# Performance work log

Hardware: AMD Instinct MI355X
Metric: run time of the kernel (lower is better)

The kernel has to match this reference:

```python
import jax, jax.numpy as jnp
import numpy as np

B, N, E = 32, 128, 16384
D, H, O, A = 72, 72, 72, 4   # n_input, n_hidden, n_output, n_node_attr
C_WEIGHT = 1.0
EPS = 1e-5  # BatchNorm1d default eps


def setup_inputs() -> dict:
    key = jax.random.key(0)
    ks = jax.random.split(key, 16)
    rn = lambda k, shp, s=0.05: jax.random.normal(k, shp, jnp.float32) * s
    return {
        "h": jax.random.normal(ks[0], (B, N, D), jnp.float32),
        "x": jax.random.normal(ks[1], (B, N, 4), jnp.float32),
        "edgei": jax.random.randint(ks[2], (B, E), 0, N),
        "edgej": jax.random.randint(ks[3], (B, E), 0, N),
        "node_attr": jax.random.normal(ks[4], (B, N, A), jnp.float32),
        # phi_e: Linear(2D+2 -> H, no bias), BN, ReLU, Linear(H->H), ReLU
        "We1": rn(ks[5], (2 * D + 2, H)),
        "g1": jnp.ones((H,), jnp.float32), "b1": jnp.zeros((H,), jnp.float32),
        "We2": rn(ks[6], (H, H)), "be2": jnp.zeros((H,), jnp.float32),
        # phi_m: Linear(H->1), Sigmoid
        "Wm": rn(ks[7], (H, 1)), "bm": jnp.zeros((1,), jnp.float32),
        # phi_x: Linear(H->H), ReLU, Linear(H->1, no bias, tiny init)
        "Wx1": rn(ks[8], (H, H)), "bx1": jnp.zeros((H,), jnp.float32),
        "Wx2": rn(ks[9], (H, 1), 0.001),
        # phi_h: Linear(H+D+A -> H), BN, ReLU, Linear(H->O)
        "Wh1": rn(ks[10], (H + D + A, H)), "bh1": jnp.zeros((H,), jnp.float32),
        "gh": jnp.ones((H,), jnp.float32), "bh": jnp.zeros((H,), jnp.float32),
        "Wh2": rn(ks[11], (H, O)), "bh2": jnp.zeros((O,), jnp.float32),
    }


def _psi(p):
    return jnp.sign(p) * jnp.log1p(jnp.abs(p))


def _normsq4(p):  # Minkowski norm: p0^2 - p1^2 - p2^2 - p3^2
    psq = p * p
    return 2.0 * psq[..., 0] - psq.sum(axis=-1)


def _dotsq4(p, q):  # Minkowski inner product
    pq = p * q
    return 2.0 * pq[..., 0] - pq.sum(axis=-1)


def _batchnorm(z, g, b):  # training-mode BatchNorm1d over flattened batch dim
    mu = z.mean(axis=0)
    var = z.var(axis=0)
    return (z - mu) * jax.lax.rsqrt(var + EPS) * g + b


_seg_sum = jax.vmap(lambda d, s: jax.ops.segment_sum(d, s, num_segments=N))


def reference(h, x, edgei, edgej, node_attr,
              We1, g1, b1, We2, be2, Wm, bm,
              Wx1, bx1, Wx2, Wh1, bh1, gh, bh, Wh2, bh2):
    # gather edge endpoint features (equiv. to torch.gather along dim 1)
    xi = jnp.take_along_axis(x, edgei[:, :, None], axis=1)    # [B,E,4]
    xj = jnp.take_along_axis(x, edgej[:, :, None], axis=1)
    hi = jnp.take_along_axis(h, edgei[:, :, None], axis=1)    # [B,E,D]
    hj = jnp.take_along_axis(h, edgej[:, :, None], axis=1)
    x_diff = xi - xj
    norms = _psi(_normsq4(x_diff))[..., None]                 # [B,E,1]
    dots = _psi(_dotsq4(xi, xj))[..., None]                   # [B,E,1]

    # m_model: phi_e then sigmoid gate phi_m
    feat = jnp.concatenate([hi, hj, norms, dots], axis=-1)    # [B,E,2D+2]
    z = feat.reshape(-1, 2 * D + 2) @ We1
    z = jax.nn.relu(_batchnorm(z, g1, b1))
    z = jax.nn.relu(z @ We2 + be2)
    m = z.reshape(B, E, H)
    m = m * jax.nn.sigmoid(m @ Wm + bm)                       # gated messages

    # x_model: equivariant coordinate update (segment mean over edges)
    gate = jax.nn.relu(m @ Wx1 + bx1) @ Wx2                   # [B,E,1]
    trans = jnp.clip(x_diff * gate, -100.0, 100.0)
    agg = _seg_sum(trans, edgei)                              # [B,N,4]
    cnt = _seg_sum(jnp.ones_like(trans), edgei)
    x_out = x + (agg / jnp.maximum(cnt, 1.0)) * C_WEIGHT

    # h_model: segment sum of messages, node MLP, residual
    magg = _seg_sum(m, edgei)                                 # [B,N,H]
    hin = jnp.concatenate([h, magg, node_attr], axis=-1).reshape(-1, H + D + A)
    z2 = hin @ Wh1 + bh1
    z2 = jax.nn.relu(_batchnorm(z2, gh, bh))
    z2 = z2 @ Wh2 + bh2
    h_out = h + z2.reshape(B, N, O)

    return (h_out, x_out, m)
```

## Files before the change

### kernel.cpp

```cpp
#include <hip/hip_runtime.h>

#define BB 32
#define NN 128
#define EE 16384
#define ROWS_E (BB*EE)
#define ROWS_N (BB*NN)
#define EPS_BN 1e-5f

#define XOUT_OFF (ROWS_N*72)
#define M_OFF    (XOUT_OFF + ROWS_N*4)

#define ST1_OFF 0
#define ST2_OFF 512
#define AGG_OFF 1024
#define CNT_OFF (AGG_OFF + ROWS_N*4)
#define MAGG_OFF (CNT_OFF + ROWS_N)
#define Z2_OFF (MAGG_OFF + ROWS_N*72)
#define ZERO_FLOATS Z2_OFF
#define WB_OFF (Z2_OFF + ROWS_N*72)

#define WE1T_OFF 0
#define WE2T_OFF 13440
#define WX1T_OFF 21760
#define WH1T_OFF 30080
#define WH2T_OFF 43520
#define WB_TOTAL 51840

typedef __attribute__((ext_vector_type(8))) short short8;
typedef __attribute__((ext_vector_type(4))) float f32x4;

__device__ __forceinline__ float psi_f(float p) {
    return copysignf(log1pf(fabsf(p)), p);
}
__device__ __forceinline__ unsigned short f2bf(float f) {
    union { float f; unsigned u; } v; v.f = f;
    unsigned r = v.u + 0x7fffu + ((v.u >> 16) & 1u);
    return (unsigned short)(r >> 16);
}
__device__ __forceinline__ unsigned pk(float a, float b) {
    return (unsigned)f2bf(a) | ((unsigned)f2bf(b) << 16);
}

__global__ void k_prep(const float* __restrict__ We1, const float* __restrict__ We2,
                       const float* __restrict__ Wx1, const float* __restrict__ Wh1,
                       const float* __restrict__ Wh2, unsigned short* __restrict__ wb)
{
    int idx = blockIdx.x * 256 + threadIdx.x;
    if (idx >= WB_TOTAL) return;
    const float* src; int off, n, k, K;
    if (idx < WE2T_OFF)      { off = idx;            n = off/168; k = off%168; src = We1; K = 146; }
    else if (idx < WH1T_OFF && idx >= WX1T_OFF) { off = idx - WX1T_OFF; n = off/104; k = off%104; src = Wx1; K = 72; }
    else if (idx < WX1T_OFF) { off = idx - WE2T_OFF; n = off/104; k = off%104; src = We2; K = 72; }
    else if (idx < WH2T_OFF) { off = idx - WH1T_OFF; n = off/168; k = off%168; src = Wh1; K = 148; }
    else                     { off = idx - WH2T_OFF; n = off/104; k = off%104; src = Wh2; K = 72; }
    float v = (n < 72 && k < K) ? src[k * 72 + n] : 0.f;
    wb[idx] = f2bf(v);
}

__global__ __launch_bounds__(256) void k_edge_gemm1(
    const float* __restrict__ h, const float* __restrict__ x,
    const int* __restrict__ ei, const int* __restrict__ ej,
    const unsigned short* __restrict__ We1t, float* __restrict__ z1)
{
    __shared__ unsigned short At[128 * 168];
    __shared__ unsigned short Wt[80 * 168];
    int tid = threadIdx.x;
    {
        const uint4* s = (const uint4*)We1t; uint4* d = (uint4*)Wt;
        for (int q = tid; q < 1680; q += 256) d[q] = s[q];
    }
    int rl = tid >> 1, half = tid & 1;
    int row = blockIdx.x * 128 + rl;
    int b = row >> 14;
    int i = ei[row], j = ej[row];
    int node = half ? j : i;
    const float4* hp = (const float4*)(h + (size_t)(b * 128 + node) * 72);
    uint2* arow = (uint2*)(&At[rl * 168 + half * 72]);
    #pragma unroll
    for (int q = 0; q < 18; q++) {
        float4 v = hp[q];
        arow[q] = make_uint2(pk(v.x, v.y), pk(v.z, v.w));
    }
    unsigned* tailp = (unsigned*)(&At[rl * 168 + 146]);
    if (half == 0) {
        float4 xi = *(const float4*)(x + (size_t)(b * 128 + i) * 4);
        float4 xj = *(const float4*)(x + (size_t)(b * 128 + j) * 4);
        float d0 = xi.x - xj.x, d1 = xi.y - xj.y, d2 = xi.z - xj.z, d3 = xi.w - xj.w;
        float nrm = d0*d0 - d1*d1 - d2*d2 - d3*d3;
        float dot = xi.x*xj.x - xi.y*xj.y - xi.z*xj.z - xi.w*xj.w;
        *(unsigned*)(&At[rl * 168 + 144]) = pk(psi_f(nrm), psi_f(dot));
        #pragma unroll
        for (int q = 0; q < 6; q++) tailp[q] = 0u;
    } else {
        #pragma unroll
        for (int q = 6; q < 11; q++) tailp[q] = 0u;
    }
    __syncthreads();

    int wv = tid >> 6, lane = tid & 63, c = lane & 15, quad = lane >> 4;
    f32x4 acc[2][5] = {};
    for (int kc = 0; kc < 5; kc++) {
        int k0 = kc * 32 + quad * 8;
        short8 a0 = *(const short8*)(&At[(wv * 32 + c) * 168 + k0]);
        short8 a1 = *(const short8*)(&At[(wv * 32 + 16 + c) * 168 + k0]);
        #pragma unroll
        for (int ct = 0; ct < 5; ct++) {
            short8 bf = *(const short8*)(&Wt[(ct * 16 + c) * 168 + k0]);
            acc[0][ct] = __builtin_amdgcn_mfma_f32_16x16x32_bf16(a0, bf, acc[0][ct], 0, 0, 0);
            acc[1][ct] = __builtin_amdgcn_mfma_f32_16x16x32_bf16(a1, bf, acc[1][ct], 0, 0, 0);
        }
    }
    size_t rbase = (size_t)blockIdx.x * 128 + wv * 32 + quad * 4;
    #pragma unroll
    for (int rt = 0; rt < 2; rt++)
        #pragma unroll
        for (int ct = 0; ct < 5; ct++) {
            int col = ct * 16 + c;
            if (col < 72) {
                float* op = z1 + (rbase + rt * 16) * 72 + col;
                #pragma unroll
                for (int r = 0; r < 4; r++) op[(size_t)r * 72] = acc[rt][ct][r];
            }
        }
}

__global__ void k_stats(const float* __restrict__ z, int rows, float* __restrict__ st)
{
    __shared__ float ssum[4][72];
    __shared__ float ssq[4][72];
    int c = threadIdx.x, ty = threadIdx.y;
    float s = 0.f, q = 0.f;
    for (int r = blockIdx.x * 4 + ty; r < rows; r += gridDim.x * 4) {
        float v = z[(size_t)r * 72 + c];
        s += v; q += v * v;
    }
    ssum[ty][c] = s; ssq[ty][c] = q;
    __syncthreads();
    if (ty == 0) {
        s = ssum[0][c] + ssum[1][c] + ssum[2][c] + ssum[3][c];
        q = ssq[0][c] + ssq[1][c] + ssq[2][c] + ssq[3][c];
        atomicAdd(&st[c], s);
        atomicAdd(&st[72 + c], q);
    }
}

__global__ void k_finalize(float* __restrict__ st, float inv_rows)
{
    int c = threadIdx.x;
    if (c < 72) {
        float mean = st[c] * inv_rows;
        float var  = st[72 + c] * inv_rows - mean * mean;
        st[144 + c] = mean;
        st[216 + c] = rsqrtf(var + EPS_BN);
    }
}

__global__ __launch_bounds__(256) void k_edge_main(
    const float* __restrict__ x, const int* __restrict__ ei, const int* __restrict__ ej,
    const float* __restrict__ st1, const float* __restrict__ g1, const float* __restrict__ b1,
    const float* __restrict__ be2, const float* __restrict__ Wm, const float* __restrict__ bm,
    const float* __restrict__ bx1, const float* __restrict__ Wx2,
    const unsigned short* __restrict__ We2t, const unsigned short* __restrict__ Wx1t,
    float* __restrict__ m, float* __restrict__ agg, float* __restrict__ cnt)
{
    __shared__ unsigned short Zt[128 * 104];
    __shared__ unsigned short W2[80 * 104];
    __shared__ unsigned short W3[80 * 104];
    __shared__ float g2buf[128];
    int tid = threadIdx.x;
    {
        const uint4* s2 = (const uint4*)We2t; uint4* d2 = (uint4*)W2;
        const uint4* s3 = (const uint4*)Wx1t; uint4* d3 = (uint4*)W3;
        for (int q = tid; q < 1040; q += 256) { d2[q] = s2[q]; d3[q] = s3[q]; }
    }
    int rl = tid >> 1, half = tid & 1;
    size_t row = (size_t)blockIdx.x * 128 + rl;
    const float* mean = st1 + 144;
    const float* inv  = st1 + 216;
    const float4* zp = (const float4*)(m + row * 72) + half * 9;
    uint2* arow = (uint2*)(&Zt[rl * 104 + half * 36]);
    #pragma unroll
    for (int q = 0; q < 9; q++) {
        int k = half * 36 + q * 4;
        float4 v = zp[q];
        float a0 = fmaxf((v.x - mean[k  ]) * inv[k  ] * g1[k  ] + b1[k  ], 0.f);
        float a1 = fmaxf((v.y - mean[k+1]) * inv[k+1] * g1[k+1] + b1[k+1], 0.f);
        float a2 = fmaxf((v.z - mean[k+2]) * inv[k+2] * g1[k+2] + b1[k+2], 0.f);
        float a3 = fmaxf((v.w - mean[k+3]) * inv[k+3] * g1[k+3] + b1[k+3], 0.f);
        arow[q] = make_uint2(pk(a0, a1), pk(a2, a3));
    }
    uint2* prow = (uint2*)(&Zt[rl * 104]);
    #pragma unroll
    for (int q = 0; q < 4; q++) prow[18 + half * 4 + q] = make_uint2(0u, 0u);
    __syncthreads();

    int wv = tid >> 6, lane = tid & 63, c = lane & 15, quad = lane >> 4;
    f32x4 acc2[2][5] = {};
    for (int kc = 0; kc < 3; kc++) {
        int k0 = kc * 32 + quad * 8;
        short8 a0 = *(const short8*)(&Zt[(wv * 32 + c) * 104 + k0]);
        short8 a1 = *(const short8*)(&Zt[(wv * 32 + 16 + c) * 104 + k0]);
        #pragma unroll
        for (int ct = 0; ct < 5; ct++) {
            short8 bf = *(const short8*)(&W2[(ct * 16 + c) * 104 + k0]);
            acc2[0][ct] = __builtin_amdgcn_mfma_f32_16x16x32_bf16(a0, bf, acc2[0][ct], 0, 0, 0);
            acc2[1][ct] = __builtin_amdgcn_mfma_f32_16x16x32_bf16(a1, bf, acc2[1][ct], 0, 0, 0);
        }
    }
    float part[2][4] = {};
    float bm0 = bm[0];
    #pragma unroll
    for (int ct = 0; ct < 5; ct++) {
        int col = ct * 16 + c;
        float bias = (col < 72) ? be2[col] : 0.f;
        float wm   = (col < 72) ? Wm[col]  : 0.f;
        #pragma unroll
        for (int rt = 0; rt < 2; rt++)
            #pragma unroll
            for (int r = 0; r < 4; r++) {
                float t = fmaxf(acc2[rt][ct][r] + bias, 0.f);
                acc2[rt][ct][r] = t;
                part[rt][r] += t * wm;
            }
    }
    float sg[2][4];
    #pragma unroll
    for (int rt = 0; rt < 2; rt++)
        #pragma unroll
        for (int r = 0; r < 4; r++) {
            float s = part[rt][r];
            s += __shfl_xor(s, 1); s += __shfl_xor(s, 2);
            s += __shfl_xor(s, 4); s += __shfl_xor(s, 8);
            sg[rt][r] = 1.f / (1.f + expf(-(s + bm0)));
        }
    size_t rbase = (size_t)blockIdx.x * 128 + wv * 32 + quad * 4;
    #pragma unroll
    for (int rt = 0; rt < 2; rt++)
        #pragma unroll
        for (int ct = 0; ct < 5; ct++) {
            int col = ct * 16 + c;
            #pragma unroll
            for (int r = 0; r < 4; r++) {
                float mv = acc2[rt][ct][r] * sg[rt][r];
                int lrow = wv * 32 + rt * 16 + quad * 4 + r;
                Zt[lrow * 104 + col] = f2bf(mv);
                if (col < 72) m[(rbase + rt * 16 + r) * 72 + col] = mv;
            }
        }
    f32x4 acc3[2][5] = {};
    for (int kc = 0; kc < 3; kc++) {
        int k0 = kc * 32 + quad * 8;
        short8 a0 = *(const short8*)(&Zt[(wv * 32 + c) * 104 + k0]);
        short8 a1 = *(const short8*)(&Zt[(wv * 32 + 16 + c) * 104 + k0]);
        #pragma unroll
        for (int ct = 0; ct < 5; ct++) {
            short8 bf = *(const short8*)(&W3[(ct * 16 + c) * 104 + k0]);
            acc3[0][ct] = __builtin_amdgcn_mfma_f32_16x16x32_bf16(a0, bf, acc3[0][ct], 0, 0, 0);
            acc3[1][ct] = __builtin_amdgcn_mfma_f32_16x16x32_bf16(a1, bf, acc3[1][ct], 0, 0, 0);
        }
    }
    float part3[2][4] = {};
    #pragma unroll
    for (int ct = 0; ct < 5; ct++) {
        int col = ct * 16 + c;
        float bias = (col < 72) ? bx1[col] : 0.f;
        float wx   = (col < 72) ? Wx2[col] : 0.f;
        #pragma unroll
        for (int rt = 0; rt < 2; rt++)
            #pragma unroll
            for (int r = 0; r < 4; r++)
                part3[rt][r] += fmaxf(acc3[rt][ct][r] + bias, 0.f) * wx;
    }
    #pragma unroll
    for (int rt = 0; rt < 2; rt++)
        #pragma unroll
        for (int r = 0; r < 4; r++) {
            float s = part3[rt][r];
            s += __shfl_xor(s, 1); s += __shfl_xor(s, 2);
            s += __shfl_xor(s, 4); s += __shfl_xor(s, 8);
            if (c == 0) g2buf[wv * 32 + rt * 16 + quad * 4 + r] = s;
        }
    __syncthreads();
    if (tid < 128) {
        size_t erow = (size_t)blockIdx.x * 128 + tid;
        int b = (int)(erow >> 14);
        int i2 = ei[erow], j2 = ej[erow];
        float g2 = g2buf[tid];
        float4 xi = *(const float4*)(x + (size_t)(b * 128 + i2) * 4);
        float4 xj = *(const float4*)(x + (size_t)(b * 128 + j2) * 4);
        float t0 = fminf(fmaxf((xi.x - xj.x) * g2, -100.f), 100.f);
        float t1 = fminf(fmaxf((xi.y - xj.y) * g2, -100.f), 100.f);
        float t2 = fminf(fmaxf((xi.z - xj.z) * g2, -100.f), 100.f);
        float t3 = fminf(fmaxf((xi.w - xj.w) * g2, -100.f), 100.f);
        float* ap = agg + (size_t)(b * 128 + i2) * 4;
        atomicAdd(ap + 0, t0); atomicAdd(ap + 1, t1);
        atomicAdd(ap + 2, t2); atomicAdd(ap + 3, t3);
        atomicAdd(cnt + (size_t)(b * 128 + i2), 1.f);
    }
}

__global__ __launch_bounds__(256) void k_magg(
    const float* __restrict__ m, const int* __restrict__ ei, float* __restrict__ magg)
{
    __shared__ float accum[128 * 72];
    int tid = threadIdx.x;
    for (int q = tid; q < 9216; q += 256) accum[q] = 0.f;
    __syncthreads();
    int b = blockIdx.x >> 3, chunk = blockIdx.x & 7;
    int wv = tid >> 6, lane = tid & 63;
    int ebase = b * 16384 + chunk * 2048;
    for (int e = wv; e < 2048; e += 4) {
        int erow = ebase + e;
        int node = ei[erow];
        const float* mr = m + (size_t)erow * 72;
        atomicAdd(&accum[node * 72 + lane], mr[lane]);
        if (lane < 8) atomicAdd(&accum[node * 72 + 64 + lane], mr[64 + lane]);
    }
    __syncthreads();
    float* mg = magg + (size_t)b * 9216;
    for (int q = tid; q < 9216; q += 256) atomicAdd(&mg[q], accum[q]);
}

__global__ __launch_bounds__(256) void k_node_gemm1(
    const float* __restrict__ h, const float* __restrict__ node_attr,
    const float* __restrict__ magg, const unsigned short* __restrict__ Wh1t,
    const float* __restrict__ bh1, float* __restrict__ z2)
{
    __shared__ unsigned short At[128 * 168];
    __shared__ unsigned short Wt[80 * 168];
    int tid = threadIdx.x;
    {
        const uint4* s = (const uint4*)Wh1t; uint4* d = (uint4*)Wt;
        for (int q = tid; q < 1680; q += 256) d[q] = s[q];
    }
    int rl = tid >> 1, half = tid & 1;
    size_t row = (size_t)blockIdx.x * 128 + rl;
    const float4* sp = (const float4*)((half ? magg : h) + row * 72);
    uint2* arow = (uint2*)(&At[rl * 168 + half * 72]);
    #pragma unroll
    for (int q = 0; q < 18; q++) {
        float4 v = sp[q];
        arow[q] = make_uint2(pk(v.x, v.y), pk(v.z, v.w));
    }
    if (half) {
        float4 na = *(const float4*)(node_attr + row * 4);
        *(unsigned*)(&At[rl * 168 + 144]) = pk(na.x, na.y);
        *(unsigned*)(&At[rl * 168 + 146]) = pk(na.z, na.w);
        unsigned* tailp = (unsigned*)(&At[rl * 168 + 148]);
        #pragma unroll
        for (int q = 0; q < 10; q++) tailp[q] = 0u;
    }
    __syncthreads();

    int wv = tid >> 6, lane = tid & 63, c = lane & 15, quad = lane >> 4;
    f32x4 acc[2][5] = {};
    for (int kc = 0; kc < 5; kc++) {
        int k0 = kc * 32 + quad * 8;
        short8 a0 = *(const short8*)(&At[(wv * 32 + c) * 168 + k0]);
        short8 a1 = *(const short8*)(&At[(wv * 32 + 16 + c) * 168 + k0]);
        #pragma unroll
        for (int ct = 0; ct < 5; ct++) {
            short8 bf = *(const short8*)(&Wt[(ct * 16 + c) * 168 + k0]);
            acc[0][ct] = __builtin_amdgcn_mfma_f32_16x16x32_bf16(a0, bf, acc[0][ct], 0, 0, 0);
            acc[1][ct] = __builtin_amdgcn_mfma_f32_16x16x32_bf16(a1, bf, acc[1][ct], 0, 0, 0);
        }
    }
    size_t rbase = (size_t)blockIdx.x * 128 + wv * 32 + quad * 4;
    #pragma unroll
    for (int rt = 0; rt < 2; rt++)
        #pragma unroll
        for (int ct = 0; ct < 5; ct++) {
            int col = ct * 16 + c;
            if (col < 72) {
                float bias = bh1[col];
                float* op = z2 + (rbase + rt * 16) * 72 + col;
                #pragma unroll
                for (int r = 0; r < 4; r++) op[(size_t)r * 72] = acc[rt][ct][r] + bias;
            }
        }
}

__global__ __launch_bounds__(256) void k_node_final(
    const float* __restrict__ h, const float* __restrict__ x,
    const float* __restrict__ z2, const float* __restrict__ st2,
    const float* __restrict__ gh, const float* __restrict__ bh,
    const unsigned short* __restrict__ Wh2t, const float* __restrict__ bh2,
    const float* __restrict__ agg, const float* __restrict__ cnt,
    float* __restrict__ hout, float* __restrict__ xout)
{
    __shared__ unsigned short Zt[128 * 104];
    __shared__ unsigned short Wt[80 * 104];
    int tid = threadIdx.x;
    {
        const uint4* s = (const uint4*)Wh2t; uint4* d = (uint4*)Wt;
        for (int q = tid; q < 1040; q += 256) d[q] = s[q];
    }
    int rl = tid >> 1, half = tid & 1;
    size_t row = (size_t)blockIdx.x * 128 + rl;
    const float* mean = st2 + 144;
    const float* inv  = st2 + 216;
    const float4* zp = (const float4*)(z2 + row * 72) + half * 9;
    uint2* arow = (uint2*)(&Zt[rl * 104 + half * 36]);
    #pragma unroll
    for (int q = 0; q < 9; q++) {
        int k = half * 36 + q * 4;
        float4 v = zp[q];
        float a0 = fmaxf((v.x - mean[k  ]) * inv[k  ] * gh[k  ] + bh[k  ], 0.f);
        float a1 = fmaxf((v.y - mean[k+1]) * inv[k+1] * gh[k+1] + bh[k+1], 0.f);
        float a2 = fmaxf((v.z - mean[k+2]) * inv[k+2] * gh[k+2] + bh[k+2], 0.f);
        float a3 = fmaxf((v.w - mean[k+3]) * inv[k+3] * gh[k+3] + bh[k+3], 0.f);
        arow[q] = make_uint2(pk(a0, a1), pk(a2, a3));
    }
    uint2* prow = (uint2*)(&Zt[rl * 104]);
    #pragma unroll
    for (int q = 0; q < 4; q++) prow[18 + half * 4 + q] = make_uint2(0u, 0u);
    __syncthreads();

    int wv = tid >> 6, lane = tid & 63, c = lane & 15, quad = lane >> 4;
    f32x4 acc[2][5] = {};
    for (int kc = 0; kc < 3; kc++) {
        int k0 = kc * 32 + quad * 8;
        short8 a0 = *(const short8*)(&Zt[(wv * 32 + c) * 104 + k0]);
        short8 a1 = *(const short8*)(&Zt[(wv * 32 + 16 + c) * 104 + k0]);
        #pragma unroll
        for (int ct = 0; ct < 5; ct++) {
            short8 bf = *(const short8*)(&Wt[(ct * 16 + c) * 104 + k0]);
            acc[0][ct] = __builtin_amdgcn_mfma_f32_16x16x32_bf16(a0, bf, acc[0][ct], 0, 0, 0);
            acc[1][ct] = __builtin_amdgcn_mfma_f32_16x16x32_bf16(a1, bf, acc[1][ct], 0, 0, 0);
        }
    }
    size_t rbase = (size_t)blockIdx.x * 128 + wv * 32 + quad * 4;
    #pragma unroll
    for (int rt = 0; rt < 2; rt++)
        #pragma unroll
        for (int ct = 0; ct < 5; ct++) {
            int col = ct * 16 + c;
            if (col < 72) {
                float bias = bh2[col];
                #pragma unroll
                for (int r = 0; r < 4; r++) {
                    size_t gr = (rbase + rt * 16 + r);
                    hout[gr * 72 + col] = h[gr * 72 + col] + acc[rt][ct][r] + bias;
                }
            }
        }
    if (tid < 128) {
        size_t nrow = (size_t)blockIdx.x * 128 + tid;
        float cn = fmaxf(cnt[nrow], 1.f);
        float4 ag = *(const float4*)(agg + nrow * 4);
        float4 xv = *(const float4*)(x + nrow * 4);
        ((float4*)xout)[nrow] = make_float4(xv.x + ag.x / cn, xv.y + ag.y / cn,
                                            xv.z + ag.z / cn, xv.w + ag.w / cn);
    }
}

extern "C" void kernel_launch(void* const* d_in, const int* in_sizes, int n_in,
                              void* d_out, int out_size, void* d_ws, size_t ws_size,
                              hipStream_t stream)
{
    const float* h   = (const float*)d_in[0];
    const float* x   = (const float*)d_in[1];
    const int*   ei  = (const int*)d_in[2];
    const int*   ej  = (const int*)d_in[3];
    const float* na  = (const float*)d_in[4];
    const float* We1 = (const float*)d_in[5];
    const float* g1  = (const float*)d_in[6];
    const float* b1  = (const float*)d_in[7];
    const float* We2 = (const float*)d_in[8];
    const float* be2 = (const float*)d_in[9];
    const float* Wm  = (const float*)d_in[10];
    const float* bm  = (const float*)d_in[11];
    const float* Wx1 = (const float*)d_in[12];
    const float* bx1 = (const float*)d_in[13];
    const float* Wx2 = (const float*)d_in[14];
    const float* Wh1 = (const float*)d_in[15];
    const float* bh1 = (const float*)d_in[16];
    const float* gh  = (const float*)d_in[17];
    const float* bhp = (const float*)d_in[18];
    const float* Wh2 = (const float*)d_in[19];
    const float* bh2 = (const float*)d_in[20];

    float* out  = (float*)d_out;
    float* hout = out;
    float* xout = out + XOUT_OFF;
    float* m    = out + M_OFF;
    float* ws   = (float*)d_ws;
    float* st1  = ws + ST1_OFF;
    float* st2  = ws + ST2_OFF;
    float* agg  = ws + AGG_OFF;
    float* cnt  = ws + CNT_OFF;
    float* magg = ws + MAGG_OFF;
    float* z2   = ws + Z2_OFF;
    unsigned short* wb = (unsigned short*)(ws + WB_OFF);

    hipMemsetAsync(d_ws, 0, (size_t)ZERO_FLOATS * sizeof(float), stream);
    k_prep<<<(WB_TOTAL + 255) / 256, 256, 0, stream>>>(We1, We2, Wx1, Wh1, Wh2, wb);
    k_edge_gemm1<<<ROWS_E / 128, 256, 0, stream>>>(h, x, ei, ej, wb + WE1T_OFF, m);
    k_stats<<<dim3(1024), dim3(72, 4), 0, stream>>>(m, ROWS_E, st1);
    k_finalize<<<1, 128, 0, stream>>>(st1, 1.0f / (float)ROWS_E);
    k_edge_main<<<ROWS_E / 128, 256, 0, stream>>>(x, ei, ej, st1, g1, b1, be2, Wm, bm,
                                                  bx1, Wx2, wb + WE2T_OFF, wb + WX1T_OFF,
                                                  m, agg, cnt);
    k_magg<<<256, 256, 0, stream>>>(m, ei, magg);
    k_node_gemm1<<<ROWS_N / 128, 256, 0, stream>>>(h, na, magg, wb + WH1T_OFF, bh1, z2);
    k_stats<<<dim3(16), dim3(72, 4), 0, stream>>>(z2, ROWS_N, st2);
    k_finalize<<<1, 128, 0, stream>>>(st2, 1.0f / (float)ROWS_N);
    k_node_final<<<ROWS_N / 128, 256, 0, stream>>>(h, x, z2, st2, gh, bhp,
                                                   wb + WH2T_OFF, bh2, agg, cnt, hout, xout);
}
```

Baseline: 776.3 us.

## Fuse BatchNorm statistics into GEMM epilogues and read weights directly from global

The per-column sum and sum-of-squares for both BatchNorms are now accumulated in the epilogues of the edge and node first-layer GEMMs. This uses wave shuffles, an LDS reduction and one atomic per column per block, which removes the separate k_stats passes that re-read the large edge activation buffer. Weight staging into LDS is dropped in the edge kernels, so MFMA operands for the weights load straight from global/L2. That shrinks LDS use, and the kernels now request three blocks per CU via launch bounds. The barrier after the A-tile fill is also removed, which relies on each wave reading only rows its own threads wrote. Global weight loads inside the MFMA loop may add latency.

Result: faster. 695.9 us (-10.4%).

```diff
diff --git a/kernel.cpp b/kernel.cpp
--- a/kernel.cpp
+++ b/kernel.cpp
@@ -57,18 +57,15 @@
     wb[idx] = f2bf(v);
 }
 
-__global__ __launch_bounds__(256) void k_edge_gemm1(
+__global__ __launch_bounds__(256, 3) void k_edge_gemm1(
     const float* __restrict__ h, const float* __restrict__ x,
     const int* __restrict__ ei, const int* __restrict__ ej,
-    const unsigned short* __restrict__ We1t, float* __restrict__ z1)
+    const unsigned short* __restrict__ We1t, float* __restrict__ z1,
+    float* __restrict__ st)
 {
     __shared__ unsigned short At[128 * 168];
-    __shared__ unsigned short Wt[80 * 168];
+    __shared__ float sred[4][144];
     int tid = threadIdx.x;
-    {
-        const uint4* s = (const uint4*)We1t; uint4* d = (uint4*)Wt;
-        for (int q = tid; q < 1680; q += 256) d[q] = s[q];
-    }
     int rl = tid >> 1, half = tid & 1;
     int row = blockIdx.x * 128 + rl;
     int b = row >> 14;
@@ -95,7 +92,6 @@
         #pragma unroll
         for (int q = 6; q < 11; q++) tailp[q] = 0u;
     }
-    __syncthreads();
 
     int wv = tid >> 6, lane = tid & 63, c = lane & 15, quad = lane >> 4;
     f32x4 acc[2][5] = {};
@@ -105,43 +101,33 @@
         short8 a1 = *(const short8*)(&At[(wv * 32 + 16 + c) * 168 + k0]);
         #pragma unroll
         for (int ct = 0; ct < 5; ct++) {
-            short8 bf = *(const short8*)(&Wt[(ct * 16 + c) * 168 + k0]);
+            short8 bf = *(const short8*)(&We1t[(ct * 16 + c) * 168 + k0]);
             acc[0][ct] = __builtin_amdgcn_mfma_f32_16x16x32_bf16(a0, bf, acc[0][ct], 0, 0, 0);
             acc[1][ct] = __builtin_amdgcn_mfma_f32_16x16x32_bf16(a1, bf, acc[1][ct], 0, 0, 0);
         }
     }
     size_t rbase = (size_t)blockIdx.x * 128 + wv * 32 + quad * 4;
     #pragma unroll
-    for (int rt = 0; rt < 2; rt++)
-        #pragma unroll
-        for (int ct = 0; ct < 5; ct++) {
-            int col = ct * 16 + c;
-            if (col < 72) {
-                float* op = z1 + (rbase + rt * 16) * 72 + col;
-                #pragma unroll
-                for (int r = 0; r < 4; r++) op[(size_t)r * 72] = acc[rt][ct][r];
+    for (int ct = 0; ct < 5; ct++) {
+        int col = ct * 16 + c;
+        float s = 0.f, q = 0.f;
+        #pragma unroll
+        for (int rt = 0; rt < 2; rt++) {
+            float* op = z1 + (rbase + rt * 16) * 72 + col;
+            #pragma unroll
+            for (int r = 0; r < 4; r++) {
+                float v = acc[rt][ct][r];
+                if (col < 72) op[(size_t)r * 72] = v;
+                s += v; q += v * v;
             }
         }
-}
-
-__global__ void k_stats(const float* __restrict__ z, int rows, float* __restrict__ st)
-{
-    __shared__ float ssum[4][72];
-    __shared__ float ssq[4][72];
-    int c = threadIdx.x, ty = threadIdx.y;
-    float s = 0.f, q = 0.f;
-    for (int r = blockIdx.x * 4 + ty; r < rows; r += gridDim.x * 4) {
-        float v = z[(size_t)r * 72 + c];
-        s += v; q += v * v;
-    }
-    ssum[ty][c] = s; ssq[ty][c] = q;
-    __syncthreads();
-    if (ty == 0) {
-        s = ssum[0][c] + ssum[1][c] + ssum[2][c] + ssum[3][c];
-        q = ssq[0][c] + ssq[1][c] + ssq[2][c] + ssq[3][c];
-        atomicAdd(&st[c], s);
-        atomicAdd(&st[72 + c], q);
-    }
+        s += __shfl_xor(s, 16); s += __shfl_xor(s, 32);
+        q += __shfl_xor(q, 16); q += __shfl_xor(q, 32);
+        if (lane < 16 && col < 72) { sred[wv][col] = s; sred[wv][72 + col] = q; }
+    }
+    __syncthreads();
+    if (tid < 144)
+        atomicAdd(&st[tid], sred[0][tid] + sred[1][tid] + sred[2][tid] + sred[3][tid]);
 }
 
 __global__ void k_finalize(float* __restrict__ st, float inv_rows)
@@ -155,7 +141,7 @@
     }
 }
 
-__global__ __launch_bounds__(256) void k_edge_main(
+__global__ __launch_bounds__(256, 3) void k_edge_main(
     const float* __restrict__ x, const int* __restrict__ ei, const int* __restrict__ ej,
     const float* __restrict__ st1, const float* __restrict__ g1, const float* __restrict__ b1,
     const float* __restrict__ be2, const float* __restrict__ Wm, const float* __restrict__ bm,
@@ -164,15 +150,8 @@
     float* __restrict__ m, float* __restrict__ agg, float* __restrict__ cnt)
 {
     __shared__ unsigned short Zt[128 * 104];
-    __shared__ unsigned short W2[80 * 104];
-    __shared__ unsigned short W3[80 * 104];
     __shared__ float g2buf[128];
     int tid = threadIdx.x;
-    {
-        const uint4* s2 = (const uint4*)We2t; uint4* d2 = (uint4*)W2;
-        const uint4* s3 = (const uint4*)Wx1t; uint4* d3 = (uint4*)W3;
-        for (int q = tid; q < 1040; q += 256) { d2[q] = s2[q]; d3[q] = s3[q]; }
-    }
     int rl = tid >> 1, half = tid & 1;
     size_t row = (size_t)blockIdx.x * 128 + rl;
     const float* mean = st1 + 144;
@@ -192,7 +171,6 @@
     uint2* prow = (uint2*)(&Zt[rl * 104]);
     #pragma unroll
     for (int q = 0; q < 4; q++) prow[18 + half * 4 + q] = make_uint2(0u, 0u);
-    __syncthreads();
 
     int wv = tid >> 6, lane = tid & 63, c = lane & 15, quad = lane >> 4;
     f32x4 acc2[2][5] = {};
@@ -202,7 +180,7 @@
         short8 a1 = *(const short8*)(&Zt[(wv * 32 + 16 + c) * 104 + k0]);
         #pragma unroll
         for (int ct = 0; ct < 5; ct++) {
-            short8 bf = *(const short8*)(&W2[(ct * 16 + c) * 104 + k0]);
+            short8 bf = *(const short8*)(&We2t[(ct * 16 + c) * 104 + k0]);
             acc2[0][ct] = __builtin_amdgcn_mfma_f32_16x16x32_bf16(a0, bf, acc2[0][ct], 0, 0, 0);
             acc2[1][ct] = __builtin_amdgcn_mfma_f32_16x16x32_bf16(a1, bf, acc2[1][ct], 0, 0, 0);
         }
@@ -254,7 +232,7 @@
         short8 a1 = *(const short8*)(&Zt[(wv * 32 + 16 + c) * 104 + k0]);
         #pragma unroll
         for (int ct = 0; ct < 5; ct++) {
-            short8 bf = *(const short8*)(&W3[(ct * 16 + c) * 104 + k0]);
+            short8 bf = *(const short8*)(&Wx1t[(ct * 16 + c) * 104 + k0]);
             acc3[0][ct] = __builtin_amdgcn_mfma_f32_16x16x32_bf16(a0, bf, acc3[0][ct], 0, 0, 0);
             acc3[1][ct] = __builtin_amdgcn_mfma_f32_16x16x32_bf16(a1, bf, acc3[1][ct], 0, 0, 0);
         }
@@ -324,10 +302,11 @@
 __global__ __launch_bounds__(256) void k_node_gemm1(
     const float* __restrict__ h, const float* __restrict__ node_attr,
     const float* __restrict__ magg, const unsigned short* __restrict__ Wh1t,
-    const float* __restrict__ bh1, float* __restrict__ z2)
+    const float* __restrict__ bh1, float* __restrict__ z2, float* __restrict__ st)
 {
     __shared__ unsigned short At[128 * 168];
     __shared__ unsigned short Wt[80 * 168];
+    __shared__ float sred[4][144];
     int tid = threadIdx.x;
     {
         const uint4* s = (const uint4*)Wh1t; uint4* d = (uint4*)Wt;
@@ -367,17 +346,27 @@
     }
     size_t rbase = (size_t)blockIdx.x * 128 + wv * 32 + quad * 4;
     #pragma unroll
-    for (int rt = 0; rt < 2; rt++)
-        #pragma unroll
-        for (int ct = 0; ct < 5; ct++) {
-            int col = ct * 16 + c;
-            if (col < 72) {
-                float bias = bh1[col];
-                float* op = z2 + (rbase + rt * 16) * 72 + col;
-                #pragma unroll
-                for (int r = 0; r < 4; r++) op[(size_t)r * 72] = acc[rt][ct][r] + bias;
+    for (int ct = 0; ct < 5; ct++) {
+        int col = ct * 16 + c;
+        float bias = (col < 72) ? bh1[col] : 0.f;
+        float s = 0.f, q = 0.f;
+        #pragma unroll
+        for (int rt = 0; rt < 2; rt++) {
+            float* op = z2 + (rbase + rt * 16) * 72 + col;
+            #pragma unroll
+            for (int r = 0; r < 4; r++) {
+                float v = acc[rt][ct][r] + bias;
+                if (col < 72) op[(size_t)r * 72] = v;
+                s += v; q += v * v;
             }
         }
+        s += __shfl_xor(s, 16); s += __shfl_xor(s, 32);
+        q += __shfl_xor(q, 16); q += __shfl_xor(q, 32);
+        if (lane < 16 && col < 72) { sred[wv][col] = s; sred[wv][72 + col] = q; }
+    }
+    __syncthreads();
+    if (tid < 144)
+        atomicAdd(&st[tid], sred[0][tid] + sred[1][tid] + sred[2][tid] + sred[3][tid]);
 }
 
 __global__ __launch_bounds__(256) void k_node_final(
@@ -495,15 +484,13 @@
 
     hipMemsetAsync(d_ws, 0, (size_t)ZERO_FLOATS * sizeof(float), stream);
     k_prep<<<(WB_TOTAL + 255) / 256, 256, 0, stream>>>(We1, We2, Wx1, Wh1, Wh2, wb);
-    k_edge_gemm1<<<ROWS_E / 128, 256, 0, stream>>>(h, x, ei, ej, wb + WE1T_OFF, m);
-    k_stats<<<dim3(1024), dim3(72, 4), 0, stream>>>(m, ROWS_E, st1);
+    k_edge_gemm1<<<ROWS_E / 128, 256, 0, stream>>>(h, x, ei, ej, wb + WE1T_OFF, m, st1);
     k_finalize<<<1, 128, 0, stream>>>(st1, 1.0f / (float)ROWS_E);
     k_edge_main<<<ROWS_E / 128, 256, 0, stream>>>(x, ei, ej, st1, g1, b1, be2, Wm, bm,
                                                   bx1, Wx2, wb + WE2T_OFF, wb + WX1T_OFF,
                                                   m, agg, cnt);
     k_magg<<<256, 256, 0, stream>>>(m, ei, magg);
-    k_node_gemm1<<<ROWS_N / 128, 256, 0, stream>>>(h, na, magg, wb + WH1T_OFF, bh1, z2);
-    k_stats<<<dim3(16), dim3(72, 4), 0, stream>>>(z2, ROWS_N, st2);
+    k_node_gemm1<<<ROWS_N / 128, 256, 0, stream>>>(h, na, magg, wb + WH1T_OFF, bh1, z2, st2);
     k_finalize<<<1, 128, 0, stream>>>(st2, 1.0f / (float)ROWS_N);
     k_node_final<<<ROWS_N / 128, 256, 0, stream>>>(h, x, z2, st2, gh, bhp,
                                                    wb + WH2T_OFF, bh2, agg, cnt, hout, xout);
```
